# Optimization experiments

Measured on AMD Instinct MI355X. Metric: run time of the kernel, lower is better.

The kernel has to match this reference:

```python
import jax, jax.numpy as jnp
import numpy as np

N = 50000      # num nodes
E = 800000     # num edges (before self-loops)
IN = 128       # in_channels
H = 8          # heads (layer 1)
C = 32         # hidden_channels per head
OUT = 64       # out_channels


def setup_inputs() -> dict:
    key = jax.random.key(0)
    ks = jax.random.split(key, 9)
    x = jax.random.normal(ks[0], (N, IN), dtype=jnp.float32)
    edge_index = jax.random.randint(ks[1], (2, E), 0, N, dtype=jnp.int64)
    # layer 1 params (heads=H, concat=True)
    W1 = jax.random.normal(ks[2], (IN, H * C), dtype=jnp.float32) / np.float32(np.sqrt(IN))
    a_src1 = jax.random.normal(ks[3], (H, C), dtype=jnp.float32) / np.float32(np.sqrt(C))
    a_dst1 = jax.random.normal(ks[4], (H, C), dtype=jnp.float32) / np.float32(np.sqrt(C))
    b1 = jnp.zeros((H * C,), dtype=jnp.float32)
    # layer 2 params (heads=1, concat=False)
    W2 = jax.random.normal(ks[5], (H * C, OUT), dtype=jnp.float32) / np.float32(np.sqrt(H * C))
    a_src2 = jax.random.normal(ks[6], (1, OUT), dtype=jnp.float32) / np.float32(np.sqrt(OUT))
    a_dst2 = jax.random.normal(ks[7], (1, OUT), dtype=jnp.float32) / np.float32(np.sqrt(OUT))
    b2 = jnp.zeros((OUT,), dtype=jnp.float32)
    return {"x": x, "edge_index": edge_index,
            "W1": W1, "a_src1": a_src1, "a_dst1": a_dst1, "b1": b1,
            "W2": W2, "a_src2": a_src2, "a_dst2": a_dst2, "b2": b2}


def _gat_layer(x, src, dst, W, a_src, a_dst, b, concat):
    # PyG GATConv (eval mode): linear -> per-head attention logits ->
    # LeakyReLU(0.2) -> segment softmax over destination -> scatter-add.
    Hh, Cc = a_src.shape
    h = (x @ W).reshape(x.shape[0], Hh, Cc)          # [N, H, C]
    al = jnp.sum(h * a_src[None], axis=-1)           # [N, H]
    ar = jnp.sum(h * a_dst[None], axis=-1)           # [N, H]
    e = jax.nn.leaky_relu(al[src] + ar[dst], 0.2)    # [E', H]
    m = jax.ops.segment_max(e, dst, num_segments=N)  # per-dst max (self-loops guarantee coverage)
    p = jnp.exp(e - m[dst])
    s = jax.ops.segment_sum(p, dst, num_segments=N)
    alpha = p / (s[dst] + 1e-16)                     # [E', H]
    out = jax.ops.segment_sum(h[src] * alpha[:, :, None], dst, num_segments=N)  # [N, H, C]
    if concat:
        return out.reshape(N, Hh * Cc) + b
    return jnp.mean(out, axis=1) + b


def reference(x, edge_index, W1, a_src1, a_dst1, b1, W2, a_src2, a_dst2, b2):
    loops = jnp.arange(N, dtype=edge_index.dtype)
    src = jnp.concatenate([edge_index[0], loops])    # add_self_loops=True
    dst = jnp.concatenate([edge_index[1], loops])
    h = _gat_layer(x, src, dst, W1, a_src1, a_dst1, b1, True)   # [N, H*C]
    h = jax.nn.elu(h)                                            # dropout inactive in eval
    return _gat_layer(h, src, dst, W2, a_src2, a_dst2, b2, False)  # [N, OUT]
```

## Files before the change

kernel.cpp:

```cpp
#include <hip/hip_runtime.h>
#include <cstdint>

#define N_NODES 50000
#define N_EDGES 800000
#define E_TOT   (N_EDGES + N_NODES)
#define IN_CH   128
#define HEADS   8
#define CCH     32
#define HC      256
#define OUTC    64

typedef unsigned short ushort_t;
typedef __attribute__((ext_vector_type(8))) short bf16x8;
typedef __attribute__((ext_vector_type(8))) unsigned short u16x8;
typedef __attribute__((ext_vector_type(4))) float f32x4;

static __device__ __forceinline__ unsigned short f2bf(float f) {
    unsigned u = __float_as_uint(f);
    u = u + 0x7fffu + ((u >> 16) & 1u);
    return (unsigned short)(u >> 16);
}
static __device__ __forceinline__ float bf2f(unsigned short h) {
    return __uint_as_float((unsigned)h << 16);
}
static __device__ __forceinline__ unsigned pack2(float lo, float hi) {
    return (unsigned)f2bf(lo) | ((unsigned)f2bf(hi) << 16);
}
static __device__ __forceinline__ float lrexp(float v) {
    v = v > 0.f ? v : 0.2f * v;
    return expf(v);
}
static __device__ __forceinline__ bf16x8 cvt8(float4 lo, float4 hi) {
    bf16x8 r;
    r[0] = (short)f2bf(lo.x); r[1] = (short)f2bf(lo.y);
    r[2] = (short)f2bf(lo.z); r[3] = (short)f2bf(lo.w);
    r[4] = (short)f2bf(hi.x); r[5] = (short)f2bf(hi.y);
    r[6] = (short)f2bf(hi.z); r[7] = (short)f2bf(hi.w);
    return r;
}

__global__ __launch_bounds__(256) void hist_kernel(
        const int* __restrict__ ei, int* __restrict__ deg) {
    int e = blockIdx.x * 256 + threadIdx.x;
    if (e >= E_TOT) return;
    int dv = (e < N_EDGES) ? ei[N_EDGES + e] : (e - N_EDGES);
    atomicAdd(&deg[dv], 1);
}

__global__ __launch_bounds__(1024) void scan1_kernel(
        const int* __restrict__ deg, int* __restrict__ inc, int* __restrict__ bsum) {
    __shared__ int sh[1024];
    const int tid = threadIdx.x;
    const int i = blockIdx.x * 1024 + tid;
    sh[tid] = (i < N_NODES) ? deg[i] : 0;
    __syncthreads();
    for (int o = 1; o < 1024; o <<= 1) {
        int t = (tid >= o) ? sh[tid - o] : 0;
        __syncthreads();
        sh[tid] += t;
        __syncthreads();
    }
    if (i < N_NODES) inc[i] = sh[tid];
    if (tid == 1023) bsum[blockIdx.x] = sh[1023];
}

#define NSCAN_BLOCKS ((N_NODES + 1023) / 1024)
__global__ __launch_bounds__(256) void finalize_kernel(
        const int* __restrict__ inc, const int* __restrict__ bsum,
        int* __restrict__ rowstart, int* __restrict__ cursor) {
    __shared__ int pref[NSCAN_BLOCKS];
    if (threadIdx.x == 0) {
        int acc = 0;
        #pragma unroll 7
        for (int k = 0; k < NSCAN_BLOCKS; ++k) { pref[k] = acc; acc += bsum[k]; }
    }
    __syncthreads();
    int i = blockIdx.x * 256 + threadIdx.x;
    if (i >= N_NODES) return;
    int v = inc[i] + pref[i >> 10];
    rowstart[i + 1] = v;
    if (i + 1 < N_NODES) cursor[i + 1] = v;
    if (i == 0) { rowstart[0] = 0; cursor[0] = 0; }
}

__global__ __launch_bounds__(256) void scatter_kernel(
        const int* __restrict__ ei, int* __restrict__ cursor, int* __restrict__ col) {
    int e = blockIdx.x * 256 + threadIdx.x;
    if (e >= E_TOT) return;
    int sv, dv;
    if (e < N_EDGES) { sv = ei[e]; dv = ei[N_EDGES + e]; }
    else             { sv = dv = e - N_EDGES; }
    int pos = atomicAdd(&cursor[dv], 1);
    col[pos] = sv;
}

__global__ __launch_bounds__(256) void repack_w(
        const float* __restrict__ W1, const float* __restrict__ W2,
        ushort_t* __restrict__ W1f, ushort_t* __restrict__ W2f) {
    int t = blockIdx.x * 256 + threadIdx.x;
    if (t < 32768) {
        int j = t & 7, lane = (t >> 3) & 63, f = t >> 9;
        int nt = f >> 2, kk = f & 3;
        int k = kk * 32 + (lane >> 4) * 8 + j;
        int n = (nt >> 1) * 32 + 2 * (lane & 15) + (nt & 1);
        W1f[t] = f2bf(W1[k * HC + n]);
    } else if (t < 32768 + 16384) {
        int u = t - 32768;
        int j = u & 7, lane = (u >> 3) & 63, f = u >> 9;
        int nt = f >> 3, kk = f & 7;
        int k = kk * 32 + (lane >> 4) * 8 + j;
        int n = (nt >> 1) * 32 + 2 * (lane & 15) + (nt & 1);
        W2f[u] = f2bf(W2[k * OUTC + n]);
    }
}

__global__ __launch_bounds__(256) void gemm1_mfma(
        const float* __restrict__ x, const ushort_t* __restrict__ W1f,
        const float* __restrict__ a_src, const float* __restrict__ a_dst,
        ushort_t* __restrict__ h1b, float* __restrict__ al, float* __restrict__ ar) {
    const int lane = threadIdx.x & 63;
    const int wv   = threadIdx.x >> 6;
    const int base = blockIdx.x * 64 + wv * 16;
    if (base >= N_NODES) return;
    const int am = base + (lane & 15);
    const int rm = am < N_NODES ? am : N_NODES - 1;

    bf16x8 a[4];
    const float* xr = &x[(size_t)rm * IN_CH + (lane >> 4) * 8];
    #pragma unroll
    for (int kk = 0; kk < 4; ++kk) {
        float4 lo = *(const float4*)&xr[kk * 32];
        float4 hi = *(const float4*)&xr[kk * 32 + 4];
        a[kk] = cvt8(lo, hi);
    }

    f32x4 acc[16];
    #pragma unroll
    for (int nt = 0; nt < 16; ++nt) acc[nt] = (f32x4){0.f, 0.f, 0.f, 0.f};

    const bf16x8* bp = (const bf16x8*)W1f;
    #pragma unroll
    for (int nt = 0; nt < 16; ++nt) {
        #pragma unroll
        for (int kk = 0; kk < 4; ++kk)
            acc[nt] = __builtin_amdgcn_mfma_f32_16x16x32_bf16(
                a[kk], bp[(nt * 4 + kk) * 64 + lane], acc[nt], 0, 0, 0);
    }

    #pragma unroll
    for (int r = 0; r < 4; ++r) {
        int node = base + (lane >> 4) * 4 + r;
        if (node < N_NODES) {
            unsigned* op = (unsigned*)&h1b[(size_t)node * HC + 2 * (lane & 15)];
            #pragma unroll
            for (int t = 0; t < 8; ++t)
                op[t * 16] = pack2(acc[2 * t][r], acc[2 * t + 1][r]);
        }
    }

    float asv[16], adv[16];
    #pragma unroll
    for (int nt = 0; nt < 16; ++nt) {
        int n = (nt >> 1) * 32 + 2 * (lane & 15) + (nt & 1);
        asv[nt] = a_src[n];
        adv[nt] = a_dst[n];
    }
    #pragma unroll
    for (int h = 0; h < HEADS; ++h) {
        #pragma unroll
        for (int r = 0; r < 4; ++r) {
            float s = acc[2 * h][r] * asv[2 * h] + acc[2 * h + 1][r] * asv[2 * h + 1];
            float d = acc[2 * h][r] * adv[2 * h] + acc[2 * h + 1][r] * adv[2 * h + 1];
            s += __shfl_xor(s, 1, 64); s += __shfl_xor(s, 2, 64);
            s += __shfl_xor(s, 4, 64); s += __shfl_xor(s, 8, 64);
            d += __shfl_xor(d, 1, 64); d += __shfl_xor(d, 2, 64);
            d += __shfl_xor(d, 4, 64); d += __shfl_xor(d, 8, 64);
            int node = base + (lane >> 4) * 4 + r;
            if ((lane & 15) == 0 && node < N_NODES) {
                al[node * HEADS + h] = s;
                ar[node * HEADS + h] = d;
            }
        }
    }
}

__global__ __launch_bounds__(256) void aggr1_csr(
        const int* __restrict__ rowstart, const int* __restrict__ col,
        const float* __restrict__ al, const float* __restrict__ ar,
        const unsigned short* __restrict__ h1b, const float* __restrict__ b1,
        unsigned short* __restrict__ out1b) {
    const int lane = threadIdx.x & 63;
    const int d = blockIdx.x * 4 + (threadIdx.x >> 6);
    if (d >= N_NODES) return;
    const int beg = rowstart[d], end = rowstart[d + 1];

    const int h8 = lane & 7;
    const float ar_h8 = ar[d * HEADS + h8];
    float denom = 0.f;
    for (int i = beg + (lane >> 3); i < end; i += 8)
        denom += lrexp(al[col[i] * HEADS + h8] + ar_h8);
    denom += __shfl_xor(denom, 8, 64);
    denom += __shfl_xor(denom, 16, 64);
    denom += __shfl_xor(denom, 32, 64);

    const int half = lane >> 5;
    const int L    = lane & 31;
    const int hh   = L >> 2;
    const float inv = 1.f / (__shfl(denom, hh, 64) + 1e-16f);
    const float ar_hh = ar[d * HEADS + hh];

    float acc8[8] = {0.f,0.f,0.f,0.f,0.f,0.f,0.f,0.f};
    int i = beg;
    for (; i + 7 < end; i += 8) {
        int sv[4]; float wv[4];
        #pragma unroll
        for (int q = 0; q < 4; ++q) sv[q] = col[i + 2 * q + half];
        #pragma unroll
        for (int q = 0; q < 4; ++q)
            wv[q] = lrexp(al[sv[q] * HEADS + hh] + ar_hh) * inv;
        #pragma unroll
        for (int q = 0; q < 4; ++q) {
            const u16x8 v = *(const u16x8*)&h1b[(size_t)sv[q] * HC + L * 8];
            #pragma unroll
            for (int j = 0; j < 8; ++j) acc8[j] += wv[q] * bf2f(v[j]);
        }
    }
    for (; i < end; i += 2) {
        const int e = i + half;
        const bool ok = e < end;
        const int s = col[ok ? e : end - 1];
        const float w = ok ? lrexp(al[s * HEADS + hh] + ar_hh) * inv : 0.f;
        const u16x8 v = *(const u16x8*)&h1b[(size_t)s * HC + L * 8];
        #pragma unroll
        for (int j = 0; j < 8; ++j) acc8[j] += w * bf2f(v[j]);
    }
    #pragma unroll
    for (int j = 0; j < 8; ++j) acc8[j] += __shfl_xor(acc8[j], 32, 64);

    if (half == 0) {
        const float4 b0 = *(const float4*)&b1[L * 8];
        const float4 b4 = *(const float4*)&b1[L * 8 + 4];
        float bb[8] = {b0.x, b0.y, b0.z, b0.w, b4.x, b4.y, b4.z, b4.w};
        u16x8 ov;
        #pragma unroll
        for (int j = 0; j < 8; ++j) {
            float v = acc8[j] + bb[j];
            v = v > 0.f ? v : expf(v) - 1.f;
            ov[j] = f2bf(v);
        }
        *(u16x8*)&out1b[(size_t)d * HC + L * 8] = ov;
    }
}

__global__ __launch_bounds__(256) void gemm2_mfma(
        const ushort_t* __restrict__ hinb, const ushort_t* __restrict__ W2f,
        const float* __restrict__ a_src, const float* __restrict__ a_dst,
        ushort_t* __restrict__ h2b, float* __restrict__ al, float* __restrict__ ar) {
    const int lane = threadIdx.x & 63;
    const int wv   = threadIdx.x >> 6;
    const int base = blockIdx.x * 64 + wv * 16;
    if (base >= N_NODES) return;
    const int am = base + (lane & 15);
    const int rm = am < N_NODES ? am : N_NODES - 1;

    bf16x8 a[8];
    const bf16x8* ap = (const bf16x8*)&hinb[(size_t)rm * HC];
    #pragma unroll
    for (int kk = 0; kk < 8; ++kk)
        a[kk] = ap[kk * 4 + (lane >> 4)];

    f32x4 acc[4];
    #pragma unroll
    for (int nt = 0; nt < 4; ++nt) acc[nt] = (f32x4){0.f, 0.f, 0.f, 0.f};

    const bf16x8* bp = (const bf16x8*)W2f;
    #pragma unroll
    for (int nt = 0; nt < 4; ++nt) {
        #pragma unroll
        for (int kk = 0; kk < 8; ++kk)
            acc[nt] = __builtin_amdgcn_mfma_f32_16x16x32_bf16(
                a[kk], bp[(nt * 8 + kk) * 64 + lane], acc[nt], 0, 0, 0);
    }

    #pragma unroll
    for (int r = 0; r < 4; ++r) {
        int node = base + (lane >> 4) * 4 + r;
        if (node < N_NODES) {
            unsigned* op = (unsigned*)&h2b[(size_t)node * OUTC + 2 * (lane & 15)];
            #pragma unroll
            for (int t = 0; t < 2; ++t)
                op[t * 16] = pack2(acc[2 * t][r], acc[2 * t + 1][r]);
        }
    }

    float asv[4], adv[4];
    #pragma unroll
    for (int nt = 0; nt < 4; ++nt) {
        int n = (nt >> 1) * 32 + 2 * (lane & 15) + (nt & 1);
        asv[nt] = a_src[n];
        adv[nt] = a_dst[n];
    }
    #pragma unroll
    for (int r = 0; r < 4; ++r) {
        float s = 0.f, d = 0.f;
        #pragma unroll
        for (int nt = 0; nt < 4; ++nt) {
            s += acc[nt][r] * asv[nt];
            d += acc[nt][r] * adv[nt];
        }
        s += __shfl_xor(s, 1, 64); s += __shfl_xor(s, 2, 64);
        s += __shfl_xor(s, 4, 64); s += __shfl_xor(s, 8, 64);
        d += __shfl_xor(d, 1, 64); d += __shfl_xor(d, 2, 64);
        d += __shfl_xor(d, 4, 64); d += __shfl_xor(d, 8, 64);
        int node = base + (lane >> 4) * 4 + r;
        if ((lane & 15) == 0 && node < N_NODES) { al[node] = s; ar[node] = d; }
    }
}

__global__ __launch_bounds__(256) void aggr2_csr(
        const int* __restrict__ rowstart, const int* __restrict__ col,
        const float* __restrict__ al, const float* __restrict__ ar,
        const unsigned short* __restrict__ h2b, const float* __restrict__ b2,
        float* __restrict__ out) {
    const int lane = threadIdx.x & 63;
    const int d = blockIdx.x * 4 + (threadIdx.x >> 6);
    if (d >= N_NODES) return;
    const int beg = rowstart[d], end = rowstart[d + 1];
    const float ard = ar[d];

    float denom = 0.f;
    for (int i = beg + lane; i < end; i += 64)
        denom += lrexp(al[col[i]] + ard);
    #pragma unroll
    for (int o = 1; o < 64; o <<= 1) denom += __shfl_xor(denom, o, 64);
    const float inv = 1.f / (denom + 1e-16f);

    const int g = lane >> 4;
    const int L = lane & 15;

    float4 acc = {0.f, 0.f, 0.f, 0.f};
    int i = beg;
    for (; i + 7 < end; i += 8) {
        const int s0 = col[i + g], s1 = col[i + 4 + g];
        const float w0 = lrexp(al[s0] + ard) * inv;
        const float w1 = lrexp(al[s1] + ard) * inv;
        const ushort4 v0 = *(const ushort4*)&h2b[(size_t)s0 * OUTC + L * 4];
        const ushort4 v1 = *(const ushort4*)&h2b[(size_t)s1 * OUTC + L * 4];
        acc.x += w0 * bf2f(v0.x) + w1 * bf2f(v1.x);
        acc.y += w0 * bf2f(v0.y) + w1 * bf2f(v1.y);
        acc.z += w0 * bf2f(v0.z) + w1 * bf2f(v1.z);
        acc.w += w0 * bf2f(v0.w) + w1 * bf2f(v1.w);
    }
    for (; i < end; i += 4) {
        const int e = i + g;
        const bool ok = e < end;
        const int s = col[ok ? e : end - 1];
        const float w = ok ? lrexp(al[s] + ard) * inv : 0.f;
        const ushort4 v = *(const ushort4*)&h2b[(size_t)s * OUTC + L * 4];
        acc.x += w * bf2f(v.x); acc.y += w * bf2f(v.y);
        acc.z += w * bf2f(v.z); acc.w += w * bf2f(v.w);
    }
    #pragma unroll
    for (int o = 16; o < 64; o <<= 1) {
        acc.x += __shfl_xor(acc.x, o, 64);
        acc.y += __shfl_xor(acc.y, o, 64);
        acc.z += __shfl_xor(acc.z, o, 64);
        acc.w += __shfl_xor(acc.w, o, 64);
    }
    if (g == 0) {
        const float4 bb = *(const float4*)&b2[L * 4];
        float4 ov = { acc.x + bb.x, acc.y + bb.y, acc.z + bb.z, acc.w + bb.w };
        *(float4*)&out[(size_t)d * OUTC + L * 4] = ov;
    }
}

extern "C" void kernel_launch(void* const* d_in, const int* in_sizes, int n_in,
                              void* d_out, int out_size, void* d_ws, size_t ws_size,
                              hipStream_t stream) {
    const float* x      = (const float*)d_in[0];
    const int*   ei     = (const int*)  d_in[1];
    const float* W1     = (const float*)d_in[2];
    const float* a_src1 = (const float*)d_in[3];
    const float* a_dst1 = (const float*)d_in[4];
    const float* b1     = (const float*)d_in[5];
    const float* W2     = (const float*)d_in[6];
    const float* a_src2 = (const float*)d_in[7];
    const float* a_dst2 = (const float*)d_in[8];
    const float* b2     = (const float*)d_in[9];
    float* out = (float*)d_out;

    char* p = (char*)d_ws;
    ushort_t* h1b   = (ushort_t*)p; p += (size_t)N_NODES * HC * 2;
    ushort_t* out1b = (ushort_t*)p; p += (size_t)N_NODES * HC * 2;
    ushort_t* h2b   = (ushort_t*)p; p += (size_t)N_NODES * OUTC * 2;
    ushort_t* W1f  = (ushort_t*)p; p += 32768 * 2;
    ushort_t* W2f  = (ushort_t*)p; p += 16384 * 2;
    float* al1  = (float*)p;  p += (size_t)N_NODES * HEADS * sizeof(float);
    float* ar1  = (float*)p;  p += (size_t)N_NODES * HEADS * sizeof(float);
    float* al2  = (float*)p;  p += (size_t)N_NODES * sizeof(float);
    float* ar2  = (float*)p;  p += (size_t)N_NODES * sizeof(float);
    int* deg      = (int*)p;  p += (size_t)N_NODES * sizeof(int);
    int* inc      = (int*)p;  p += (size_t)N_NODES * sizeof(int);
    int* bsum     = (int*)p;  p += (size_t)NSCAN_BLOCKS * sizeof(int);
    int* rowstart = (int*)p;  p += (size_t)(N_NODES + 1) * sizeof(int);
    int* cursor   = (int*)p;  p += (size_t)N_NODES * sizeof(int);
    int* col      = (int*)p;  p += (size_t)E_TOT * sizeof(int);

    hipMemsetAsync(deg, 0, (size_t)N_NODES * sizeof(int), stream);
    repack_w       <<<192, 256, 0, stream>>>(W1, W2, W1f, W2f);
    hist_kernel    <<<(E_TOT + 255)/256, 256, 0, stream>>>(ei, deg);
    scan1_kernel   <<<NSCAN_BLOCKS, 1024, 0, stream>>>(deg, inc, bsum);
    finalize_kernel<<<(N_NODES + 255)/256, 256, 0, stream>>>(inc, bsum, rowstart, cursor);
    scatter_kernel <<<(E_TOT + 255)/256, 256, 0, stream>>>(ei, cursor, col);

    gemm1_mfma <<<(N_NODES + 63)/64, 256, 0, stream>>>(x, W1f, a_src1, a_dst1, h1b, al1, ar1);
    aggr1_csr  <<<(N_NODES + 3)/4, 256, 0, stream>>>(rowstart, col, al1, ar1, h1b, b1, out1b);

    gemm2_mfma <<<(N_NODES + 63)/64, 256, 0, stream>>>(out1b, W2f, a_src2, a_dst2, h2b, al2, ar2);
    aggr2_csr  <<<(N_NODES + 3)/4, 256, 0, stream>>>(rowstart, col, al2, ar2, h2b, b2, out);
}
```

Measured before the change: 266.6 us.

## Split softmax into alpha kernels that store per-edge exp values

Each aggregation kernel is split in two. A new alpha kernel computes the per-edge exponentiated logits once, stores them (bf16 for layer 1, fp32 for layer 2) along with the per-node inverse denominator, and the aggregation kernel reads them instead of recomputing exp and gathering al[src]. This removes the repeated random gather of al and the second exp pass, but it adds extra kernel launches and writes and re-reads a per-edge buffer. The layer-1 weights also lose precision because they are rounded to bf16.

Result: slower. 272.0 us (+2.0%).

```diff
diff --git a/kernel.cpp b/kernel.cpp
--- a/kernel.cpp
+++ b/kernel.cpp
@@ -184,30 +184,42 @@
     }
 }
 
-__global__ __launch_bounds__(256) void aggr1_csr(
+__global__ __launch_bounds__(256) void alpha1_csr(
         const int* __restrict__ rowstart, const int* __restrict__ col,
         const float* __restrict__ al, const float* __restrict__ ar,
-        const unsigned short* __restrict__ h1b, const float* __restrict__ b1,
-        unsigned short* __restrict__ out1b) {
+        ushort_t* __restrict__ expv, float* __restrict__ inv1) {
     const int lane = threadIdx.x & 63;
     const int d = blockIdx.x * 4 + (threadIdx.x >> 6);
     if (d >= N_NODES) return;
     const int beg = rowstart[d], end = rowstart[d + 1];
-
     const int h8 = lane & 7;
     const float ar_h8 = ar[d * HEADS + h8];
     float denom = 0.f;
-    for (int i = beg + (lane >> 3); i < end; i += 8)
-        denom += lrexp(al[col[i] * HEADS + h8] + ar_h8);
+    for (int i = beg + (lane >> 3); i < end; i += 8) {
+        float e = lrexp(al[col[i] * HEADS + h8] + ar_h8);
+        expv[(size_t)i * 8 + h8] = f2bf(e);
+        denom += e;
+    }
     denom += __shfl_xor(denom, 8, 64);
     denom += __shfl_xor(denom, 16, 64);
     denom += __shfl_xor(denom, 32, 64);
+    if (lane < 8) inv1[d * HEADS + lane] = 1.f / (denom + 1e-16f);
+}
+
+__global__ __launch_bounds__(256) void aggr1_csr(
+        const int* __restrict__ rowstart, const int* __restrict__ col,
+        const ushort_t* __restrict__ expv, const float* __restrict__ inv1,
+        const unsigned short* __restrict__ h1b, const float* __restrict__ b1,
+        unsigned short* __restrict__ out1b) {
+    const int lane = threadIdx.x & 63;
+    const int d = blockIdx.x * 4 + (threadIdx.x >> 6);
+    if (d >= N_NODES) return;
+    const int beg = rowstart[d], end = rowstart[d + 1];
 
     const int half = lane >> 5;
     const int L    = lane & 31;
     const int hh   = L >> 2;
-    const float inv = 1.f / (__shfl(denom, hh, 64) + 1e-16f);
-    const float ar_hh = ar[d * HEADS + hh];
+    const float inv = inv1[d * HEADS + hh];
 
     float acc8[8] = {0.f,0.f,0.f,0.f,0.f,0.f,0.f,0.f};
     int i = beg;
@@ -217,7 +229,7 @@
         for (int q = 0; q < 4; ++q) sv[q] = col[i + 2 * q + half];
         #pragma unroll
         for (int q = 0; q < 4; ++q)
-            wv[q] = lrexp(al[sv[q] * HEADS + hh] + ar_hh) * inv;
+            wv[q] = bf2f(expv[(size_t)(i + 2 * q + half) * 8 + hh]) * inv;
         #pragma unroll
         for (int q = 0; q < 4; ++q) {
             const u16x8 v = *(const u16x8*)&h1b[(size_t)sv[q] * HC + L * 8];
@@ -229,7 +241,7 @@
         const int e = i + half;
         const bool ok = e < end;
         const int s = col[ok ? e : end - 1];
-        const float w = ok ? lrexp(al[s * HEADS + hh] + ar_hh) * inv : 0.f;
+        const float w = ok ? bf2f(expv[(size_t)e * 8 + hh]) * inv : 0.f;
         const u16x8 v = *(const u16x8*)&h1b[(size_t)s * HC + L * 8];
         #pragma unroll
         for (int j = 0; j < 8; ++j) acc8[j] += w * bf2f(v[j]);
@@ -317,23 +329,36 @@
     }
 }
 
-__global__ __launch_bounds__(256) void aggr2_csr(
+__global__ __launch_bounds__(256) void alpha2_csr(
         const int* __restrict__ rowstart, const int* __restrict__ col,
         const float* __restrict__ al, const float* __restrict__ ar,
-        const unsigned short* __restrict__ h2b, const float* __restrict__ b2,
-        float* __restrict__ out) {
+        float* __restrict__ expv, float* __restrict__ inv2) {
     const int lane = threadIdx.x & 63;
     const int d = blockIdx.x * 4 + (threadIdx.x >> 6);
     if (d >= N_NODES) return;
     const int beg = rowstart[d], end = rowstart[d + 1];
     const float ard = ar[d];
-
     float denom = 0.f;
-    for (int i = beg + lane; i < end; i += 64)
-        denom += lrexp(al[col[i]] + ard);
+    for (int i = beg + lane; i < end; i += 64) {
+        float e = lrexp(al[col[i]] + ard);
+        expv[i] = e;
+        denom += e;
+    }
     #pragma unroll
     for (int o = 1; o < 64; o <<= 1) denom += __shfl_xor(denom, o, 64);
-    const float inv = 1.f / (denom + 1e-16f);
+    if (lane == 0) inv2[d] = 1.f / (denom + 1e-16f);
+}
+
+__global__ __launch_bounds__(256) void aggr2_csr(
+        const int* __restrict__ rowstart, const int* __restrict__ col,
+        const float* __restrict__ expv, const float* __restrict__ inv2,
+        const unsigned short* __restrict__ h2b, const float* __restrict__ b2,
+        float* __restrict__ out) {
+    const int lane = threadIdx.x & 63;
+    const int d = blockIdx.x * 4 + (threadIdx.x >> 6);
+    if (d >= N_NODES) return;
+    const int beg = rowstart[d], end = rowstart[d + 1];
+    const float inv = inv2[d];
 
     const int g = lane >> 4;
     const int L = lane & 15;
@@ -342,8 +367,7 @@
     int i = beg;
     for (; i + 7 < end; i += 8) {
         const int s0 = col[i + g], s1 = col[i + 4 + g];
-        const float w0 = lrexp(al[s0] + ard) * inv;
-        const float w1 = lrexp(al[s1] + ard) * inv;
+        const float w0 = expv[i + g] * inv, w1 = expv[i + 4 + g] * inv;
         const ushort4 v0 = *(const ushort4*)&h2b[(size_t)s0 * OUTC + L * 4];
         const ushort4 v1 = *(const ushort4*)&h2b[(size_t)s1 * OUTC + L * 4];
         acc.x += w0 * bf2f(v0.x) + w1 * bf2f(v1.x);
@@ -355,7 +379,7 @@
         const int e = i + g;
         const bool ok = e < end;
         const int s = col[ok ? e : end - 1];
-        const float w = ok ? lrexp(al[s] + ard) * inv : 0.f;
+        const float w = ok ? expv[e] * inv : 0.f;
         const ushort4 v = *(const ushort4*)&h2b[(size_t)s * OUTC + L * 4];
         acc.x += w * bf2f(v.x); acc.y += w * bf2f(v.y);
         acc.z += w * bf2f(v.z); acc.w += w * bf2f(v.w);
@@ -393,12 +417,16 @@
     ushort_t* h1b   = (ushort_t*)p; p += (size_t)N_NODES * HC * 2;
     ushort_t* out1b = (ushort_t*)p; p += (size_t)N_NODES * HC * 2;
     ushort_t* h2b   = (ushort_t*)p; p += (size_t)N_NODES * OUTC * 2;
+    ushort_t* expv1 = (ushort_t*)p; p += (size_t)E_TOT * 8 * 2;
+    float* expv2 = (float*)p; p += (size_t)E_TOT * sizeof(float);
     ushort_t* W1f  = (ushort_t*)p; p += 32768 * 2;
     ushort_t* W2f  = (ushort_t*)p; p += 16384 * 2;
     float* al1  = (float*)p;  p += (size_t)N_NODES * HEADS * sizeof(float);
     float* ar1  = (float*)p;  p += (size_t)N_NODES * HEADS * sizeof(float);
+    float* inv1 = (float*)p;  p += (size_t)N_NODES * HEADS * sizeof(float);
     float* al2  = (float*)p;  p += (size_t)N_NODES * sizeof(float);
     float* ar2  = (float*)p;  p += (size_t)N_NODES * sizeof(float);
+    float* inv2 = (float*)p;  p += (size_t)N_NODES * sizeof(float);
     int* deg      = (int*)p;  p += (size_t)N_NODES * sizeof(int);
     int* inc      = (int*)p;  p += (size_t)N_NODES * sizeof(int);
     int* bsum     = (int*)p;  p += (size_t)NSCAN_BLOCKS * sizeof(int);
@@ -414,8 +442,10 @@
     scatter_kernel <<<(E_TOT + 255)/256, 256, 0, stream>>>(ei, cursor, col);
 
     gemm1_mfma <<<(N_NODES + 63)/64, 256, 0, stream>>>(x, W1f, a_src1, a_dst1, h1b, al1, ar1);
-    aggr1_csr  <<<(N_NODES + 3)/4, 256, 0, stream>>>(rowstart, col, al1, ar1, h1b, b1, out1b);
+    alpha1_csr <<<(N_NODES + 3)/4, 256, 0, stream>>>(rowstart, col, al1, ar1, expv1, inv1);
+    aggr1_csr  <<<(N_NODES + 3)/4, 256, 0, stream>>>(rowstart, col, expv1, inv1, h1b, b1, out1b);
 
     gemm2_mfma <<<(N_NODES + 63)/64, 256, 0, stream>>>(out1b, W2f, a_src2, a_dst2, h2b, al2, ar2);
-    aggr2_csr  <<<(N_NODES + 3)/4, 256, 0, stream>>>(rowstart, col, al2, ar2, h2b, b2, out);
-}
+    alpha2_csr <<<(N_NODES + 3)/4, 256, 0, stream>>>(rowstart, col, al2, ar2, expv2, inv2);
+    aggr2_csr  <<<(N_NODES + 3)/4, 256, 0, stream>>>(rowstart, col, expv2, inv2, h2b, b2, out);
+}
```

## Single-pass softmax aggregation with shuffled weights; fuse weight repack into histogram

Applied to the files above, without the earlier changes.

Both aggregation kernels now compute the softmax denominator in the same pass as the weighted feature accumulation. Each lane computes one exp per edge-head, and source indices and weights are broadcast with wave shuffles. Normalisation by the denominator is deferred to the end, which removes the separate gather pass over col and al and the duplicated exp work. The weight repack kernel is merged into the degree histogram kernel to save a launch. The aggregation loops now handle edges in chunks of 8 with masked tails, so short rows do some wasted work.

Result: faster. 254.1 us (-4.7%).

```diff
diff --git a/kernel.cpp b/kernel.cpp
--- a/kernel.cpp
+++ b/kernel.cpp
@@ -39,62 +39,8 @@
     return r;
 }
 
-__global__ __launch_bounds__(256) void hist_kernel(
-        const int* __restrict__ ei, int* __restrict__ deg) {
-    int e = blockIdx.x * 256 + threadIdx.x;
-    if (e >= E_TOT) return;
-    int dv = (e < N_EDGES) ? ei[N_EDGES + e] : (e - N_EDGES);
-    atomicAdd(&deg[dv], 1);
-}
-
-__global__ __launch_bounds__(1024) void scan1_kernel(
-        const int* __restrict__ deg, int* __restrict__ inc, int* __restrict__ bsum) {
-    __shared__ int sh[1024];
-    const int tid = threadIdx.x;
-    const int i = blockIdx.x * 1024 + tid;
-    sh[tid] = (i < N_NODES) ? deg[i] : 0;
-    __syncthreads();
-    for (int o = 1; o < 1024; o <<= 1) {
-        int t = (tid >= o) ? sh[tid - o] : 0;
-        __syncthreads();
-        sh[tid] += t;
-        __syncthreads();
-    }
-    if (i < N_NODES) inc[i] = sh[tid];
-    if (tid == 1023) bsum[blockIdx.x] = sh[1023];
-}
-
-#define NSCAN_BLOCKS ((N_NODES + 1023) / 1024)
-__global__ __launch_bounds__(256) void finalize_kernel(
-        const int* __restrict__ inc, const int* __restrict__ bsum,
-        int* __restrict__ rowstart, int* __restrict__ cursor) {
-    __shared__ int pref[NSCAN_BLOCKS];
-    if (threadIdx.x == 0) {
-        int acc = 0;
-        #pragma unroll 7
-        for (int k = 0; k < NSCAN_BLOCKS; ++k) { pref[k] = acc; acc += bsum[k]; }
-    }
-    __syncthreads();
-    int i = blockIdx.x * 256 + threadIdx.x;
-    if (i >= N_NODES) return;
-    int v = inc[i] + pref[i >> 10];
-    rowstart[i + 1] = v;
-    if (i + 1 < N_NODES) cursor[i + 1] = v;
-    if (i == 0) { rowstart[0] = 0; cursor[0] = 0; }
-}
-
-__global__ __launch_bounds__(256) void scatter_kernel(
-        const int* __restrict__ ei, int* __restrict__ cursor, int* __restrict__ col) {
-    int e = blockIdx.x * 256 + threadIdx.x;
-    if (e >= E_TOT) return;
-    int sv, dv;
-    if (e < N_EDGES) { sv = ei[e]; dv = ei[N_EDGES + e]; }
-    else             { sv = dv = e - N_EDGES; }
-    int pos = atomicAdd(&cursor[dv], 1);
-    col[pos] = sv;
-}
-
-__global__ __launch_bounds__(256) void repack_w(
+__global__ __launch_bounds__(256) void prep_kernel(
+        const int* __restrict__ ei, int* __restrict__ deg,
         const float* __restrict__ W1, const float* __restrict__ W2,
         ushort_t* __restrict__ W1f, ushort_t* __restrict__ W2f) {
     int t = blockIdx.x * 256 + threadIdx.x;
@@ -112,6 +58,57 @@
         int n = (nt >> 1) * 32 + 2 * (lane & 15) + (nt & 1);
         W2f[u] = f2bf(W2[k * OUTC + n]);
     }
+    if (t < E_TOT) {
+        int dv = (t < N_EDGES) ? ei[N_EDGES + t] : (t - N_EDGES);
+        atomicAdd(&deg[dv], 1);
+    }
+}
+
+__global__ __launch_bounds__(1024) void scan1_kernel(
+        const int* __restrict__ deg, int* __restrict__ inc, int* __restrict__ bsum) {
+    __shared__ int sh[1024];
+    const int tid = threadIdx.x;
+    const int i = blockIdx.x * 1024 + tid;
+    sh[tid] = (i < N_NODES) ? deg[i] : 0;
+    __syncthreads();
+    for (int o = 1; o < 1024; o <<= 1) {
+        int t = (tid >= o) ? sh[tid - o] : 0;
+        __syncthreads();
+        sh[tid] += t;
+        __syncthreads();
+    }
+    if (i < N_NODES) inc[i] = sh[tid];
+    if (tid == 1023) bsum[blockIdx.x] = sh[1023];
+}
+
+#define NSCAN_BLOCKS ((N_NODES + 1023) / 1024)
+__global__ __launch_bounds__(256) void finalize_kernel(
+        const int* __restrict__ inc, const int* __restrict__ bsum,
+        int* __restrict__ rowstart, int* __restrict__ cursor) {
+    __shared__ int pref[NSCAN_BLOCKS];
+    if (threadIdx.x == 0) {
+        int acc = 0;
+        #pragma unroll 7
+        for (int k = 0; k < NSCAN_BLOCKS; ++k) { pref[k] = acc; acc += bsum[k]; }
+    }
+    __syncthreads();
+    int i = blockIdx.x * 256 + threadIdx.x;
+    if (i >= N_NODES) return;
+    int v = inc[i] + pref[i >> 10];
+    rowstart[i + 1] = v;
+    if (i + 1 < N_NODES) cursor[i + 1] = v;
+    if (i == 0) { rowstart[0] = 0; cursor[0] = 0; }
+}
+
+__global__ __launch_bounds__(256) void scatter_kernel(
+        const int* __restrict__ ei, int* __restrict__ cursor, int* __restrict__ col) {
+    int e = blockIdx.x * 256 + threadIdx.x;
+    if (e >= E_TOT) return;
+    int sv, dv;
+    if (e < N_EDGES) { sv = ei[e]; dv = ei[N_EDGES + e]; }
+    else             { sv = dv = e - N_EDGES; }
+    int pos = atomicAdd(&cursor[dv], 1);
+    col[pos] = sv;
 }
 
 __global__ __launch_bounds__(256) void gemm1_mfma(
@@ -194,46 +191,37 @@
     if (d >= N_NODES) return;
     const int beg = rowstart[d], end = rowstart[d + 1];
 
-    const int h8 = lane & 7;
-    const float ar_h8 = ar[d * HEADS + h8];
-    float denom = 0.f;
-    for (int i = beg + (lane >> 3); i < end; i += 8)
-        denom += lrexp(al[col[i] * HEADS + h8] + ar_h8);
-    denom += __shfl_xor(denom, 8, 64);
-    denom += __shfl_xor(denom, 16, 64);
-    denom += __shfl_xor(denom, 32, 64);
-
+    const int eq = lane >> 3;
+    const int eh = lane & 7;
+    const float ar_eh = ar[d * HEADS + eh];
     const int half = lane >> 5;
     const int L    = lane & 31;
     const int hh   = L >> 2;
-    const float inv = 1.f / (__shfl(denom, hh, 64) + 1e-16f);
-    const float ar_hh = ar[d * HEADS + hh];
-
+
+    float dsum = 0.f;
     float acc8[8] = {0.f,0.f,0.f,0.f,0.f,0.f,0.f,0.f};
-    int i = beg;
-    for (; i + 7 < end; i += 8) {
-        int sv[4]; float wv[4];
-        #pragma unroll
-        for (int q = 0; q < 4; ++q) sv[q] = col[i + 2 * q + half];
-        #pragma unroll
-        for (int q = 0; q < 4; ++q)
-            wv[q] = lrexp(al[sv[q] * HEADS + hh] + ar_hh) * inv;
+
+    for (int i = beg; i < end; i += 8) {
+        const int e = i + eq;
+        const int sv_e = col[e < end ? e : end - 1];
+        const float ex = (e < end) ? lrexp(al[sv_e * HEADS + eh] + ar_eh) : 0.f;
+        dsum += ex;
         #pragma unroll
         for (int q = 0; q < 4; ++q) {
-            const u16x8 v = *(const u16x8*)&h1b[(size_t)sv[q] * HC + L * 8];
+            const int src = (2 * q + half) * 8;
+            const int   sq = __shfl(sv_e, src, 64);
+            const float wq = __shfl(ex, src + hh, 64);
+            const u16x8 v = *(const u16x8*)&h1b[(size_t)sq * HC + L * 8];
             #pragma unroll
-            for (int j = 0; j < 8; ++j) acc8[j] += wv[q] * bf2f(v[j]);
-        }
-    }
-    for (; i < end; i += 2) {
-        const int e = i + half;
-        const bool ok = e < end;
-        const int s = col[ok ? e : end - 1];
-        const float w = ok ? lrexp(al[s * HEADS + hh] + ar_hh) * inv : 0.f;
-        const u16x8 v = *(const u16x8*)&h1b[(size_t)s * HC + L * 8];
-        #pragma unroll
-        for (int j = 0; j < 8; ++j) acc8[j] += w * bf2f(v[j]);
-    }
+            for (int j = 0; j < 8; ++j) acc8[j] += wq * bf2f(v[j]);
+        }
+    }
+    dsum += __shfl_xor(dsum, 8, 64);
+    dsum += __shfl_xor(dsum, 16, 64);
+    dsum += __shfl_xor(dsum, 32, 64);
+    const float inv = 1.f / (__shfl(dsum, hh, 64) + 1e-16f);
+    #pragma unroll
+    for (int j = 0; j < 8; ++j) acc8[j] *= inv;
     #pragma unroll
     for (int j = 0; j < 8; ++j) acc8[j] += __shfl_xor(acc8[j], 32, 64);
 
@@ -328,38 +316,33 @@
     const int beg = rowstart[d], end = rowstart[d + 1];
     const float ard = ar[d];
 
-    float denom = 0.f;
-    for (int i = beg + lane; i < end; i += 64)
-        denom += lrexp(al[col[i]] + ard);
-    #pragma unroll
-    for (int o = 1; o < 64; o <<= 1) denom += __shfl_xor(denom, o, 64);
-    const float inv = 1.f / (denom + 1e-16f);
-
-    const int g = lane >> 4;
-    const int L = lane & 15;
-
+    const int e8 = lane & 7;
+    const int g  = lane >> 4;
+    const int L  = lane & 15;
+
+    float dsum = 0.f;
     float4 acc = {0.f, 0.f, 0.f, 0.f};
-    int i = beg;
-    for (; i + 7 < end; i += 8) {
-        const int s0 = col[i + g], s1 = col[i + 4 + g];
-        const float w0 = lrexp(al[s0] + ard) * inv;
-        const float w1 = lrexp(al[s1] + ard) * inv;
-        const ushort4 v0 = *(const ushort4*)&h2b[(size_t)s0 * OUTC + L * 4];
-        const ushort4 v1 = *(const ushort4*)&h2b[(size_t)s1 * OUTC + L * 4];
-        acc.x += w0 * bf2f(v0.x) + w1 * bf2f(v1.x);
-        acc.y += w0 * bf2f(v0.y) + w1 * bf2f(v1.y);
-        acc.z += w0 * bf2f(v0.z) + w1 * bf2f(v1.z);
-        acc.w += w0 * bf2f(v0.w) + w1 * bf2f(v1.w);
-    }
-    for (; i < end; i += 4) {
-        const int e = i + g;
-        const bool ok = e < end;
-        const int s = col[ok ? e : end - 1];
-        const float w = ok ? lrexp(al[s] + ard) * inv : 0.f;
-        const ushort4 v = *(const ushort4*)&h2b[(size_t)s * OUTC + L * 4];
-        acc.x += w * bf2f(v.x); acc.y += w * bf2f(v.y);
-        acc.z += w * bf2f(v.z); acc.w += w * bf2f(v.w);
-    }
+
+    for (int i = beg; i < end; i += 8) {
+        const int e = i + e8;
+        const int sv_e = col[e < end ? e : end - 1];
+        const float ex = (e < end) ? lrexp(al[sv_e] + ard) : 0.f;
+        dsum += ex;
+        #pragma unroll
+        for (int q = 0; q < 2; ++q) {
+            const int slot = q * 4 + g;
+            const int   sq = __shfl(sv_e, slot, 64);
+            const float wq = __shfl(ex, slot, 64);
+            const ushort4 v = *(const ushort4*)&h2b[(size_t)sq * OUTC + L * 4];
+            acc.x += wq * bf2f(v.x); acc.y += wq * bf2f(v.y);
+            acc.z += wq * bf2f(v.z); acc.w += wq * bf2f(v.w);
+        }
+    }
+    dsum += __shfl_xor(dsum, 1, 64);
+    dsum += __shfl_xor(dsum, 2, 64);
+    dsum += __shfl_xor(dsum, 4, 64);
+    const float inv = 1.f / (dsum + 1e-16f);
+    acc.x *= inv; acc.y *= inv; acc.z *= inv; acc.w *= inv;
     #pragma unroll
     for (int o = 16; o < 64; o <<= 1) {
         acc.x += __shfl_xor(acc.x, o, 64);
@@ -407,8 +390,7 @@
     int* col      = (int*)p;  p += (size_t)E_TOT * sizeof(int);
 
     hipMemsetAsync(deg, 0, (size_t)N_NODES * sizeof(int), stream);
-    repack_w       <<<192, 256, 0, stream>>>(W1, W2, W1f, W2f);
-    hist_kernel    <<<(E_TOT + 255)/256, 256, 0, stream>>>(ei, deg);
+    prep_kernel    <<<(E_TOT + 255)/256, 256, 0, stream>>>(ei, deg, W1, W2, W1f, W2f);
     scan1_kernel   <<<NSCAN_BLOCKS, 1024, 0, stream>>>(deg, inc, bsum);
     finalize_kernel<<<(N_NODES + 255)/256, 256, 0, stream>>>(inc, bsum, rowstart, cursor);
     scatter_kernel <<<(E_TOT + 255)/256, 256, 0, stream>>>(ei, cursor, col);
```
